# Optimization experiments

Measured on AMD Instinct MI355X. Metric: run time of the kernel, lower is better.

## Reference

```python
import jax, jax.numpy as jnp
import numpy as np

REL_SIZE = 65
TAG_SIZE = 4


def _rope(y):
    # Interleaved rotary position embedding, matching the torch module:
    # cos_pos = cos(theta) repeat_interleave(2), sin_pos = sin(theta) repeat_interleave(2)
    # y2 = (-y1, y0, -y3, y2, ...)
    B, S, H = y.shape
    half = H // 2
    pos = jnp.arange(S, dtype=jnp.float32)[:, None]                      # (S,1)
    inv_freq = jnp.power(10000.0, -2.0 * jnp.arange(half, dtype=jnp.float32) / H)
    theta = pos * inv_freq                                               # (S, half)
    cos = jnp.repeat(jnp.cos(theta), 2, axis=-1)                          # (S, H)
    sin = jnp.repeat(jnp.sin(theta), 2, axis=-1)                          # (S, H)
    yr = y.reshape(B, S, half, 2)
    y2 = jnp.stack([-yr[..., 1], yr[..., 0]], axis=-1).reshape(B, S, H)
    return y * cos + y2 * sin


def setup_inputs() -> dict:
    key = jax.random.key(0)
    k1, k2, k3 = jax.random.split(key, 3)
    B, S, H = 1, 160, 768
    y = jax.random.normal(k1, (B, S, H), dtype=jnp.float32)
    event_idx = jax.random.randint(k2, (B, 16), 0, S)
    W1 = jax.random.normal(k3, (H, 2 * H), dtype=jnp.float32) * 0.02
    b1 = jnp.zeros((H,), dtype=jnp.float32)
    W2 = jax.random.normal(jax.random.fold_in(key, 7), (REL_SIZE * TAG_SIZE, H), dtype=jnp.float32) * 0.02
    b2 = jnp.zeros((REL_SIZE * TAG_SIZE,), dtype=jnp.float32)
    return {"y": y, "event_idx": event_idx, "W1": W1, "b1": b1, "W2": W2, "b2": b2}


def reference(y, event_idx, W1, b1, W2, b2):
    # Eval path (training=False): event_idx unused, dropout = identity, sigmoid applied.
    B, S, H = y.shape
    yrot = _rope(y)
    # Linear(cat(a, b)) is separable: split W1 into the halves acting on a and b.
    Wa, Wb = W1[:, :H], W1[:, H:]
    left = jnp.einsum('bsh,oh->bso', yrot, Wa)                  # contribution of token i (row)
    right = jnp.einsum('bsh,oh->bso', yrot, Wb) + b1            # contribution of token j (col)
    h = jax.nn.relu(left[:, :, None, :] + right[:, None, :, :])  # (B, S, S, H)
    out = jnp.einsum('bijh,oh->bijo', h, W2) + b2               # (B, S, S, 260)
    out = out.reshape(B, S, S, REL_SIZE, TAG_SIZE).transpose(0, 3, 1, 2, 4)  # (B, 65, S, S, 4)
    return jax.nn.sigmoid(out)
```

## Files before the change

kernel.cpp:

```cpp
#include <hip/hip_runtime.h>
#include <hip/hip_bf16.h>
#include <cstdint>

#define SDIM 160
#define HDIM 768
#define HALF 384
#define ODIM 260
#define OPAD 272
#define CHUNK_BYTES 34816
#define WS_SMALL 1155088
#define WS_BIG   3514384

typedef __attribute__((ext_vector_type(8))) short short8;
typedef __attribute__((ext_vector_type(4))) float floatx4;
typedef _Float16 half8 __attribute__((ext_vector_type(8)));

typedef const __attribute__((address_space(1))) unsigned char gl_u8;
typedef __attribute__((address_space(3))) unsigned char lds_u8;

static __device__ __forceinline__ float bf2f(unsigned short u) {
    union { unsigned int i; float f; } v; v.i = ((unsigned int)u) << 16; return v.f;
}
static __device__ __forceinline__ unsigned short f2bf(float x) {
    __hip_bfloat16 h = __float2bfloat16(x);
    return *reinterpret_cast<unsigned short*>(&h);
}
static __device__ __forceinline__ unsigned short f2h(float x) {
    _Float16 h = (_Float16)x;
    return *reinterpret_cast<unsigned short*>(&h);
}
static __device__ __forceinline__ float q(float x) { return bf2f(f2bf(x)); }

__global__ __launch_bounds__(256) void prep_kernel(
    const float* __restrict__ y, const float* __restrict__ W1,
    const float* __restrict__ W2,
    unsigned short* __restrict__ yb, unsigned short* __restrict__ W2b,
    unsigned short* __restrict__ W1b, int do_w1b) {
    int bid = blockIdx.x;
    int t = threadIdx.x;
    if (bid < SDIM) {
        int s = bid;
        for (int p = t; p < HALF; p += 256) {
            float invf = __expf(-(2.0f * (float)p / (float)HDIM) * 9.210340371976184f);
            float th = (float)s * invf;
            float c = cosf(th), sn = sinf(th);
            float y0 = y[s * HDIM + 2 * p], y1 = y[s * HDIM + 2 * p + 1];
            yb[s * HDIM + 2 * p]     = f2bf(y0 * c - y1 * sn);
            yb[s * HDIM + 2 * p + 1] = f2bf(y1 * c + y0 * sn);
        }
    } else if (bid < SDIM + 102) {
        int idx = (bid - SDIM) * 256 + t;
        if (idx < 96 * OPAD) {
            int kg = idx / OPAD, row = idx - kg * OPAD;
            unsigned short o8[8];
            if (row < ODIM) {
                float4 a = *reinterpret_cast<const float4*>(W2 + row * HDIM + kg * 8);
                float4 b = *reinterpret_cast<const float4*>(W2 + row * HDIM + kg * 8 + 4);
                o8[0] = f2h(a.x); o8[1] = f2h(a.y); o8[2] = f2h(a.z); o8[3] = f2h(a.w);
                o8[4] = f2h(b.x); o8[5] = f2h(b.y); o8[6] = f2h(b.z); o8[7] = f2h(b.w);
            } else {
                #pragma unroll
                for (int e = 0; e < 8; ++e) o8[e] = 0;
            }
            *reinterpret_cast<uint4*>(W2b + ((size_t)kg * OPAD + row) * 8) =
                *reinterpret_cast<uint4*>(o8);
        }
    } else if (do_w1b) {
        int idx = (bid - SDIM - 102) * 256 + t;
        int kg = idx / 1536, row = idx - kg * 1536;
        const float* src = (row < 768) ? (W1 + row * 1536 + kg * 8)
                                       : (W1 + (row - 768) * 1536 + 768 + kg * 8);
        float4 a = *reinterpret_cast<const float4*>(src);
        float4 b = *reinterpret_cast<const float4*>(src + 4);
        unsigned short o8[8];
        o8[0] = f2bf(a.x); o8[1] = f2bf(a.y); o8[2] = f2bf(a.z); o8[3] = f2bf(a.w);
        o8[4] = f2bf(b.x); o8[5] = f2bf(b.y); o8[6] = f2bf(b.z); o8[7] = f2bf(b.w);
        *reinterpret_cast<uint4*>(W1b + ((size_t)kg * 1536 + row) * 8) =
            *reinterpret_cast<uint4*>(o8);
    }
}

__global__ __launch_bounds__(64, 2) void lr3_kernel(
    const unsigned short* __restrict__ yb, const unsigned short* __restrict__ W1b,
    const float* __restrict__ b1,
    unsigned short* __restrict__ Lb, unsigned short* __restrict__ Rt) {
    int l = threadIdx.x & 63;
    int l16 = l & 15, qd = l >> 4;
    int mt = blockIdx.x;
    int sq = blockIdx.y;
    int s0 = sq * 16 + l16;

    floatx4 acc = (floatx4){0.0f, 0.0f, 0.0f, 0.0f};

    const unsigned short* yrow0 = yb + s0 * HDIM;

    for (int ks = 0; ks < 24; ++ks) {
        int k = ks * 32 + qd * 8;
        int kg = ks * 4 + qd;
        union { uint4 u; short8 s; } bu0, au;
        bu0.u = *reinterpret_cast<const uint4*>(yrow0 + k);
        au.u = *reinterpret_cast<const uint4*>(
            W1b + ((size_t)kg * 1536 + mt * 16 + l16) * 8);
        acc = __builtin_amdgcn_mfma_f32_16x16x32_bf16(
            au.s, bu0.s, acc, 0, 0, 0);
    }

    int o2 = mt * 16 + qd * 4;
    int s_out = sq * 16 + l16;
    unsigned short out4[4];
    if (o2 < 768) {
        #pragma unroll
        for (int r = 0; r < 4; ++r) out4[r] = f2h(acc[r]);
        *reinterpret_cast<uint2*>(Lb + s_out * HDIM + o2) =
            *reinterpret_cast<uint2*>(out4);
    } else {
        int ob = o2 - 768;
        #pragma unroll
        for (int r = 0; r < 4; ++r)
            out4[r] = f2h(acc[r] + b1[ob + r]);
        *reinterpret_cast<uint2*>(
            Rt + ((size_t)(ob >> 3) * SDIM + s_out) * 8 + (ob & 7)) =
            *reinterpret_cast<uint2*>(out4);
    }
}

__global__ __launch_bounds__(256) void lr_fallback_kernel(
    const unsigned short* __restrict__ yb, const float* __restrict__ W1,
    const float* __restrict__ b1,
    unsigned short* __restrict__ Lb, unsigned short* __restrict__ Rt) {
    int idx = blockIdx.x * 256 + threadIdx.x;
    int s = idx / 1536;
    int o2 = idx - s * 1536;
    const unsigned short* yrow = yb + s * HDIM;
    if (o2 < 768) {
        const float* wp = W1 + o2 * 1536;
        float a0 = 0.0f;
        for (int k = 0; k < HDIM; ++k) a0 += q(wp[k]) * bf2f(yrow[k]);
        Lb[s * HDIM + o2] = f2h(a0);
    } else {
        int ob = o2 - 768;
        const float* wp = W1 + ob * 1536 + 768;
        float a0 = 0.0f;
        for (int k = 0; k < HDIM; ++k) a0 += q(wp[k]) * bf2f(yrow[k]);
        Rt[((size_t)(ob >> 3) * SDIM + s) * 8 + (ob & 7)] = f2h(a0 + b1[ob]);
    }
}

__global__ __launch_bounds__(512) void main_kernel(
    const unsigned short* __restrict__ Lb, const unsigned short* __restrict__ Rt,
    const unsigned short* __restrict__ W2b,
    const float* __restrict__ b2, float* __restrict__ out) {
    __shared__ __align__(16) unsigned char lds[3 * CHUNK_BYTES];

    int w = threadIdx.x >> 6;
    int l = threadIdx.x & 63;
    int l16 = l & 15, qd = l >> 4;
    int jh = w & 1;
    int mq = w >> 1;
    int mt0 = mq * 4;
    int nmt = (mq == 3) ? 5 : 4;
    int i0 = blockIdx.x * 2;
    int j = blockIdx.y * 32 + jh * 16 + l16;

    floatx4 acc[2][5];
    #pragma unroll
    for (int c = 0; c < 2; ++c)
        #pragma unroll
        for (int mtl = 0; mtl < 5; ++mtl)
            acc[c][mtl] = (floatx4){0.0f, 0.0f, 0.0f, 0.0f};

    const unsigned short* Lrow0 = Lb + i0 * HDIM;
    const unsigned short* Lrow1 = Lb + (i0 + 1) * HDIM;
    const unsigned char* wsrc = reinterpret_cast<const unsigned char*>(W2b);

    auto STAGE = [&](int ch) {
        const unsigned char* gsrc = wsrc + ch * CHUNK_BYTES;
        unsigned char* ldst = lds + (ch % 3) * CHUNK_BYTES;
        #pragma unroll
        for (int it = 0; it < 5; ++it) {
            int seg = w + it * 8;
            if (seg < 34) {
                __builtin_amdgcn_global_load_lds(
                    (gl_u8*)(gsrc + seg * 1024 + l * 16),
                    (lds_u8*)(ldst + seg * 1024), 16, 0, 0);
            }
        }
    };

    STAGE(0);
    STAGE(1);

    for (int kc = 0; kc < 12; ++kc) {
        if (kc == 11) {
            asm volatile("s_waitcnt vmcnt(0)" ::: "memory");
        } else if (w < 2) {
            asm volatile("s_waitcnt vmcnt(5)" ::: "memory");
        } else {
            asm volatile("s_waitcnt vmcnt(4)" ::: "memory");
        }
        __builtin_amdgcn_s_barrier();
        if (kc < 10) STAGE(kc + 2);

        int bufbase = (kc % 3) * CHUNK_BYTES;
        #pragma unroll
        for (int ks = 0; ks < 2; ++ks) {
            int k = kc * 64 + ks * 32 + qd * 8;
            int kg = kc * 8 + ks * 4 + qd;
            half8 bfrag[2];
            union { uint4 u; half8 h; } ru;
            ru.u = *reinterpret_cast<const uint4*>(
                Rt + ((size_t)kg * SDIM + j) * 8);
            #pragma unroll
            for (int c = 0; c < 2; ++c) {
                const unsigned short* Lr = c ? Lrow1 : Lrow0;
                union { uint4 u; half8 h; } lu;
                lu.u = *reinterpret_cast<const uint4*>(Lr + k);
                half8 hv = lu.h + ru.h;
                #pragma unroll
                for (int e = 0; e < 8; ++e)
                    hv[e] = hv[e] > (_Float16)0.0f ? hv[e] : (_Float16)0.0f;
                bfrag[c] = hv;
            }
            int ldsbase = bufbase + ((ks * 4 + qd) * OPAD + l16) * 16;
            #pragma unroll
            for (int mtl = 0; mtl < 5; ++mtl) {
                if (mtl < nmt) {
                    union { uint4 u; half8 h; } au;
                    au.u = *reinterpret_cast<const uint4*>(
                        lds + ldsbase + (mt0 + mtl) * 256);
                    acc[0][mtl] = __builtin_amdgcn_mfma_f32_16x16x32_f16(
                        au.h, bfrag[0], acc[0][mtl], 0, 0, 0);
                    acc[1][mtl] = __builtin_amdgcn_mfma_f32_16x16x32_f16(
                        au.h, bfrag[1], acc[1][mtl], 0, 0, 0);
                }
            }
        }
    }

    #pragma unroll
    for (int c = 0; c < 2; ++c) {
        int i = i0 + c;
        #pragma unroll
        for (int mtl = 0; mtl < 5; ++mtl) {
            if (mtl < nmt) {
                int ob = (mt0 + mtl) * 16 + qd * 4;
                if (ob < ODIM) {
                    float4 bv = *reinterpret_cast<const float4*>(b2 + ob);
                    int rel = ob >> 2;
                    float4 v;
                    v.x = 1.0f / (1.0f + __expf(-(acc[c][mtl][0] + bv.x)));
                    v.y = 1.0f / (1.0f + __expf(-(acc[c][mtl][1] + bv.y)));
                    v.z = 1.0f / (1.0f + __expf(-(acc[c][mtl][2] + bv.z)));
                    v.w = 1.0f / (1.0f + __expf(-(acc[c][mtl][3] + bv.w)));
                    *reinterpret_cast<float4*>(
                        out + (((rel * SDIM) + i) * SDIM + j) * 4) = v;
                }
            }
        }
    }
}

__global__ void ws_too_small_kernel(float* out) { out[0] = 999.0f; }

extern "C" void kernel_launch(void* const* d_in, const int* in_sizes, int n_in,
                              void* d_out, int out_size, void* d_ws, size_t ws_size,
                              hipStream_t stream) {
    const float* y  = (const float*)d_in[0];
    const float* W1 = (const float*)d_in[2];
    const float* b1 = (const float*)d_in[3];
    const float* W2 = (const float*)d_in[4];
    const float* b2 = (const float*)d_in[5];
    float* out = (float*)d_out;

    if (ws_size < (size_t)WS_SMALL) {
        ws_too_small_kernel<<<dim3(1), dim3(1), 0, stream>>>(out);
        return;
    }

    unsigned short* yb  = (unsigned short*)((char*)d_ws + 16);
    unsigned short* Lb  = yb + SDIM * HDIM;
    unsigned short* Rt  = Lb + SDIM * HDIM;
    unsigned short* W2b = Rt + SDIM * HDIM;
    unsigned short* W1b = W2b + 96 * OPAD * 8;

    if (ws_size >= (size_t)WS_BIG) {
        prep_kernel<<<dim3(SDIM + 102 + 576), dim3(256), 0, stream>>>(
            y, W1, W2, yb, W2b, W1b, 1);
        lr3_kernel<<<dim3(96, 10), dim3(64), 0, stream>>>(yb, W1b, b1, Lb, Rt);
        main_kernel<<<dim3(80, 5), dim3(512), 0, stream>>>(Lb, Rt, W2b, b2, out);
    } else {
        prep_kernel<<<dim3(SDIM + 102), dim3(256), 0, stream>>>(
            y, W1, W2, yb, W2b, W1b, 0);
        lr_fallback_kernel<<<dim3(960), dim3(256), 0, stream>>>(yb, W1, b1, Lb, Rt);
        main_kernel<<<dim3(80, 5), dim3(512), 0, stream>>>(Lb, Rt, W2b, b2, out);
    }
}
```

Measured before the change: 123.4 us.

## Split main kernel into single-wave blocks reading W2 directly from global

The main kernel drops the triple-buffered LDS staging of W2 chunks (global_load_lds with waitcnt and barriers). Each of the 8 waves becomes its own 64-thread block, indexed by blockIdx.z, and reads its W2 fragments straight from global memory, relying on L1/L2 caching. This removes the barrier synchronisation and the LDS footprint, which should allow more concurrent blocks. In exchange W2 is no longer shared across waves through LDS, so global and cache traffic per MFMA rises and load latency is no longer explicitly prefetched.

Result: no change. 122.7 us (-0.6%).

```diff
diff --git a/kernel.cpp b/kernel.cpp
--- a/kernel.cpp
+++ b/kernel.cpp
@@ -7,16 +7,12 @@
 #define HALF 384
 #define ODIM 260
 #define OPAD 272
-#define CHUNK_BYTES 34816
 #define WS_SMALL 1155088
 #define WS_BIG   3514384
 
 typedef __attribute__((ext_vector_type(8))) short short8;
 typedef __attribute__((ext_vector_type(4))) float floatx4;
 typedef _Float16 half8 __attribute__((ext_vector_type(8)));
-
-typedef const __attribute__((address_space(1))) unsigned char gl_u8;
-typedef __attribute__((address_space(3))) unsigned char lds_u8;
 
 static __device__ __forceinline__ float bf2f(unsigned short u) {
     union { unsigned int i; float f; } v; v.i = ((unsigned int)u) << 16; return v.f;
@@ -146,15 +142,13 @@
     }
 }
 
-__global__ __launch_bounds__(512) void main_kernel(
+__global__ __launch_bounds__(64, 4) void main_kernel(
     const unsigned short* __restrict__ Lb, const unsigned short* __restrict__ Rt,
     const unsigned short* __restrict__ W2b,
     const float* __restrict__ b2, float* __restrict__ out) {
-    __shared__ __align__(16) unsigned char lds[3 * CHUNK_BYTES];
-
-    int w = threadIdx.x >> 6;
     int l = threadIdx.x & 63;
     int l16 = l & 15, qd = l >> 4;
+    int w = blockIdx.z;
     int jh = w & 1;
     int mq = w >> 1;
     int mt0 = mq * 4;
@@ -171,37 +165,10 @@
 
     const unsigned short* Lrow0 = Lb + i0 * HDIM;
     const unsigned short* Lrow1 = Lb + (i0 + 1) * HDIM;
-    const unsigned char* wsrc = reinterpret_cast<const unsigned char*>(W2b);
-
-    auto STAGE = [&](int ch) {
-        const unsigned char* gsrc = wsrc + ch * CHUNK_BYTES;
-        unsigned char* ldst = lds + (ch % 3) * CHUNK_BYTES;
-        #pragma unroll
-        for (int it = 0; it < 5; ++it) {
-            int seg = w + it * 8;
-            if (seg < 34) {
-                __builtin_amdgcn_global_load_lds(
-                    (gl_u8*)(gsrc + seg * 1024 + l * 16),
-                    (lds_u8*)(ldst + seg * 1024), 16, 0, 0);
-            }
-        }
-    };
-
-    STAGE(0);
-    STAGE(1);
-
+    const unsigned short* wbase = W2b + (size_t)l16 * 8;
+
+    #pragma unroll 2
     for (int kc = 0; kc < 12; ++kc) {
-        if (kc == 11) {
-            asm volatile("s_waitcnt vmcnt(0)" ::: "memory");
-        } else if (w < 2) {
-            asm volatile("s_waitcnt vmcnt(5)" ::: "memory");
-        } else {
-            asm volatile("s_waitcnt vmcnt(4)" ::: "memory");
-        }
-        __builtin_amdgcn_s_barrier();
-        if (kc < 10) STAGE(kc + 2);
-
-        int bufbase = (kc % 3) * CHUNK_BYTES;
         #pragma unroll
         for (int ks = 0; ks < 2; ++ks) {
             int k = kc * 64 + ks * 32 + qd * 8;
@@ -221,13 +188,13 @@
                     hv[e] = hv[e] > (_Float16)0.0f ? hv[e] : (_Float16)0.0f;
                 bfrag[c] = hv;
             }
-            int ldsbase = bufbase + ((ks * 4 + qd) * OPAD + l16) * 16;
+            const unsigned short* wkg = wbase + (size_t)kg * OPAD * 8;
             #pragma unroll
             for (int mtl = 0; mtl < 5; ++mtl) {
                 if (mtl < nmt) {
                     union { uint4 u; half8 h; } au;
                     au.u = *reinterpret_cast<const uint4*>(
-                        lds + ldsbase + (mt0 + mtl) * 256);
+                        wkg + (size_t)(mt0 + mtl) * 16 * 8);
                     acc[0][mtl] = __builtin_amdgcn_mfma_f32_16x16x32_f16(
                         au.h, bfrag[0], acc[0][mtl], 0, 0, 0);
                     acc[1][mtl] = __builtin_amdgcn_mfma_f32_16x16x32_f16(
@@ -287,11 +254,11 @@
         prep_kernel<<<dim3(SDIM + 102 + 576), dim3(256), 0, stream>>>(
             y, W1, W2, yb, W2b, W1b, 1);
         lr3_kernel<<<dim3(96, 10), dim3(64), 0, stream>>>(yb, W1b, b1, Lb, Rt);
-        main_kernel<<<dim3(80, 5), dim3(512), 0, stream>>>(Lb, Rt, W2b, b2, out);
+        main_kernel<<<dim3(80, 5, 8), dim3(64), 0, stream>>>(Lb, Rt, W2b, b2, out);
     } else {
         prep_kernel<<<dim3(SDIM + 102), dim3(256), 0, stream>>>(
             y, W1, W2, yb, W2b, W1b, 0);
         lr_fallback_kernel<<<dim3(960), dim3(256), 0, stream>>>(yb, W1, b1, Lb, Rt);
-        main_kernel<<<dim3(80, 5), dim3(512), 0, stream>>>(Lb, Rt, W2b, b2, out);
-    }
-}
+        main_kernel<<<dim3(80, 5, 8), dim3(64), 0, stream>>>(Lb, Rt, W2b, b2, out);
+    }
+}
```
